# Performance work log

Hardware: AMD Instinct MI355X
Metric: run time of the kernel (lower is better)

The kernel has to match this reference:

```python
import jax, jax.numpy as jnp
import numpy as np

RNN = 400
K_WIN = 10      # num_window_mixtures
N_MIX = 20      # num_mixtures
ALPHA = 80      # alphabet_size
IN2 = RNN + ALPHA + 3  # lstm2/lstm3 input size = 483
MDN_OUT = 1 + 6 * N_MIX  # 121


def setup_inputs() -> dict:
    key = jax.random.key(0)
    ks = jax.random.split(key, 20)
    std = 0.075
    B, T, U = 256, 800, 100
    inp = {
        "trajectory": jax.random.normal(ks[0], (B, T, 3), jnp.float32),
        "char_sequence": jax.random.uniform(ks[1], (B, U, ALPHA), jnp.float32),
        # LSTM1 (input 3)
        "w_ih1": jax.random.normal(ks[2], (4 * RNN, 3), jnp.float32) * std,
        "w_hh1": jax.random.normal(ks[3], (4 * RNN, RNN), jnp.float32) * std,
        "b1": jax.random.normal(ks[4], (4 * RNN,), jnp.float32) * std,
        # LSTM2 (input 483)
        "w_ih2": jax.random.normal(ks[5], (4 * RNN, IN2), jnp.float32) * std,
        "w_hh2": jax.random.normal(ks[6], (4 * RNN, RNN), jnp.float32) * std,
        "b2": jax.random.normal(ks[7], (4 * RNN,), jnp.float32) * std,
        # LSTM3 (input 483)
        "w_ih3": jax.random.normal(ks[8], (4 * RNN, IN2), jnp.float32) * std,
        "w_hh3": jax.random.normal(ks[9], (4 * RNN, RNN), jnp.float32) * std,
        "b3": jax.random.normal(ks[10], (4 * RNN,), jnp.float32) * std,
        # window linear (Graves attention), bias init mean -3.0 std 0.25
        "w_win": jax.random.normal(ks[11], (3 * K_WIN, RNN), jnp.float32) * std,
        "b_win": jax.random.normal(ks[12], (3 * K_WIN,), jnp.float32) * 0.25 - 3.0,
        # MDN head
        "w_mdn": jax.random.normal(ks[13], (MDN_OUT, RNN), jnp.float32) * std,
        "b_mdn": jax.random.normal(ks[14], (MDN_OUT,), jnp.float32) * std,
    }
    return inp


def _lstm_cell(x, h, c, w_ih, w_hh, b):
    # torch.nn.LSTMCell gate order: i, f, g, o
    gates = x @ w_ih.T + h @ w_hh.T + b
    i, f, g, o = jnp.split(gates, 4, axis=-1)
    c_new = jax.nn.sigmoid(f) * c + jax.nn.sigmoid(i) * jnp.tanh(g)
    h_new = jax.nn.sigmoid(o) * jnp.tanh(c_new)
    return h_new, c_new


def reference(trajectory, char_sequence,
              w_ih1, w_hh1, b1, w_ih2, w_hh2, b2, w_ih3, w_hh3, b3,
              w_win, b_win, w_mdn, b_mdn):
    B, T, _ = trajectory.shape
    U = char_sequence.shape[1]
    u = jnp.arange(U, dtype=trajectory.dtype)  # [U]

    def step(carry, x_t):
        h1, c1, h2, c2, h3, c3, kappa = carry
        h1, c1 = _lstm_cell(x_t, h1, c1, w_ih1, w_hh1, b1)
        # Gaussian-window attention
        wp = jnp.exp(h1 @ w_win.T + b_win).reshape(B, 3, K_WIN)
        alpha, beta, dkappa = wp[:, 0], wp[:, 1], wp[:, 2]
        kappa = kappa + dkappa
        # phi: [B, U] = sum_k alpha_k * exp(-beta_k * (kappa_k - u)^2)
        diff = kappa[:, :, None] - u[None, None, :]          # [B, K, U]
        phi = jnp.sum(alpha[:, :, None] * jnp.exp(-beta[:, :, None] * diff * diff), axis=1)
        window = jnp.einsum('bu,bua->ba', phi, char_sequence)  # [B, ALPHA]
        x2 = jnp.concatenate([h1, window, x_t], axis=1)
        h2, c2 = _lstm_cell(x2, h2, c2, w_ih2, w_hh2, b2)
        x3 = jnp.concatenate([h2, window, x_t], axis=1)
        h3, c3 = _lstm_cell(x3, h3, c3, w_ih3, w_hh3, b3)
        out = h3 @ w_mdn.T + b_mdn  # [B, 121]
        return (h1, c1, h2, c2, h3, c3, kappa), out

    z = jnp.zeros((B, RNN), trajectory.dtype)
    kappa0 = jnp.zeros((B, K_WIN), trajectory.dtype)
    carry0 = (z, z, z, z, z, z, kappa0)
    _, outs = jax.lax.scan(step, carry0, jnp.swapaxes(trajectory, 0, 1))  # [T, B, 121]
    return jnp.swapaxes(outs, 0, 1)  # [B, T, 121]
```

## Files before the change

### kernel.cpp

```cpp
#include <hip/hip_runtime.h>
#include <hip/hip_bf16.h>

#define RNNU 400
#define NBATCH 256
#define TT 800
#define UU 100
#define ALW 80
#define KW 10
#define K1 416
#define K2 896
#define NBLK 96
#define NTHR 256

typedef unsigned short u16;
typedef unsigned int u32;
typedef unsigned long long u64;
typedef __attribute__((ext_vector_type(8))) short bfrag;
typedef __attribute__((ext_vector_type(4))) float f4;

constexpr long P1 = (long)NBATCH * K1;
constexpr long P2 = (long)NBATCH * K2;
constexpr long WP1 = 1600L * K1;
constexpr long WP2 = 1600L * K2;
constexpr long WPM = 128L * K1;
constexpr long WPW = 32L * K1;

constexpr size_t OFF_FLAGS = 0;
constexpr size_t OFF_U1 = 16384;
constexpr size_t OFF_U2 = OFF_U1 + (size_t)4 * P1 * 2;
constexpr size_t OFF_U3 = OFF_U2 + (size_t)4 * P2 * 2;
constexpr size_t OFF_W1 = OFF_U3 + (size_t)4 * P2 * 2;
constexpr size_t OFF_W2 = OFF_W1 + (size_t)2 * WP1 * 2;
constexpr size_t OFF_W3 = OFF_W2 + (size_t)2 * WP2 * 2;
constexpr size_t OFF_WM = OFF_W3 + (size_t)2 * WP2 * 2;
constexpr size_t OFF_WW = OFF_WM + (size_t)2 * WPM * 2;
constexpr size_t OFF_PB1 = OFF_WW + (size_t)2 * WPW * 2;
constexpr size_t OFF_PB2 = OFF_PB1 + 6400;
constexpr size_t OFF_PB3 = OFF_PB2 + 6400;
constexpr size_t OFF_C1 = OFF_PB3 + 6400;
constexpr size_t OFF_C2 = OFF_C1 + 409600;
constexpr size_t OFF_C3 = OFF_C2 + 409600;
constexpr size_t OFF_KP = OFF_C3 + 409600;

__device__ __forceinline__ u16 f2b(float x) {
  union { float f; u32 u; } v; v.f = x;
  u32 r = (v.u + 0x7FFFu + ((v.u >> 16) & 1u)) >> 16;
  return (u16)r;
}
__device__ __forceinline__ float b2f(u16 h) {
  union { u32 u; float f; } q; q.u = ((u32)h) << 16; return q.f;
}
__device__ __forceinline__ void wsp2(u16* base, long plane, long idx, float v) {
  u16 hi = f2b(v);
  base[idx] = hi;
  base[plane + idx] = f2b(v - b2f(hi));
}
__device__ __forceinline__ void wsp2c(u16* base, long plane, long idx, float v) {
  u16 hi = f2b(v);
  __hip_atomic_store(base + idx, hi, __ATOMIC_RELAXED, __HIP_MEMORY_SCOPE_AGENT);
  __hip_atomic_store(base + plane + idx, f2b(v - b2f(hi)), __ATOMIC_RELAXED, __HIP_MEMORY_SCOPE_AGENT);
}
__device__ __forceinline__ void st_coh16(u16* p, u16 v) {
  __hip_atomic_store(p, v, __ATOMIC_RELAXED, __HIP_MEMORY_SCOPE_AGENT);
}
__device__ __forceinline__ bfrag ld_frag_coh(const u16* p) {
  u64 lo = __hip_atomic_load((const u64*)p, __ATOMIC_RELAXED, __HIP_MEMORY_SCOPE_AGENT);
  u64 hi = __hip_atomic_load((const u64*)(p + 4), __ATOMIC_RELAXED, __HIP_MEMORY_SCOPE_AGENT);
  union { u64 q[2]; bfrag f; } u; u.q[0] = lo; u.q[1] = hi; return u.f;
}
__device__ __forceinline__ float sigf(float x) { return 1.f / (1.f + __expf(-x)); }
__device__ __forceinline__ float tanhf_(float x) {
  float e = __expf(-2.f * x); return (1.f - e) / (1.f + e);
}

__global__ void prep_kernel(
    const float* __restrict__ w_ih1, const float* __restrict__ w_hh1, const float* __restrict__ b1,
    const float* __restrict__ w_ih2, const float* __restrict__ w_hh2, const float* __restrict__ b2,
    const float* __restrict__ w_ih3, const float* __restrict__ w_hh3, const float* __restrict__ b3,
    const float* __restrict__ w_win, const float* __restrict__ w_mdn,
    const float* __restrict__ traj, char* __restrict__ ws)
{
  u16* W1 = (u16*)(ws + OFF_W1);
  u16* W2 = (u16*)(ws + OFF_W2);
  u16* W3 = (u16*)(ws + OFF_W3);
  u16* WM = (u16*)(ws + OFF_WM);
  u16* WW = (u16*)(ws + OFF_WW);

  const long N1 = WP1, N2 = WP2, N3 = WP2;
  const long N4 = WPM, N5 = WPW, N6 = 4800, N7 = 307200, N8 = 2560, N9 = 4096;
  const long N10 = P1, N11 = (long)NBATCH * RNNU, N12 = (long)NBATCH * RNNU;
  const long total = N1 + N2 + N3 + N4 + N5 + N6 + N7 + N8 + N9 + N10 + N11 + N12;

  for (long i = (long)blockIdx.x * blockDim.x + threadIdx.x; i < total;
       i += (long)gridDim.x * blockDim.x) {
    long j = i;
    if (j < N1) { int n = (int)(j / K1), k = (int)(j % K1);
      int s = (n & 3) * 400 + (n >> 2);
      float v = (k < 3) ? w_ih1[s * 3 + k] : ((k >= 16) ? w_hh1[(long)s * 400 + (k - 16)] : 0.f);
      wsp2(W1, WP1, j, v); continue; } j -= N1;
    if (j < N2) { int n = (int)(j / K2), k = (int)(j % K2);
      int s = (n & 3) * 400 + (n >> 2);
      float v = (k < 483) ? w_ih2[(long)s * 483 + k] : ((k >= 496) ? w_hh2[(long)s * 400 + (k - 496)] : 0.f);
      wsp2(W2, WP2, j, v); continue; } j -= N2;
    if (j < N3) { int n = (int)(j / K2), k = (int)(j % K2);
      int s = (n & 3) * 400 + (n >> 2);
      float v = (k < 483) ? w_ih3[(long)s * 483 + k] : ((k >= 496) ? w_hh3[(long)s * 400 + (k - 496)] : 0.f);
      wsp2(W3, WP2, j, v); continue; } j -= N3;
    if (j < N4) { int n = (int)(j / K1), k = (int)(j % K1);
      float v = (n < 121 && k >= 16) ? w_mdn[(long)n * 400 + (k - 16)] : 0.f;
      wsp2(WM, WPM, j, v); continue; } j -= N4;
    if (j < N5) { int n = (int)(j / K1), k = (int)(j % K1);
      float v = (n < 30 && k < 400) ? w_win[(long)n * 400 + k] : 0.f;
      wsp2(WW, WPW, j, v); continue; } j -= N5;
    if (j < N6) { int w = (int)(j / 1600), n = (int)(j % 1600);
      int s = (n & 3) * 400 + (n >> 2);
      float* pb = (float*)(ws + (w == 0 ? OFF_PB1 : (w == 1 ? OFF_PB2 : OFF_PB3)));
      const float* bb = (w == 0 ? b1 : (w == 1 ? b2 : b3));
      pb[n] = bb[s]; continue; } j -= N6;
    if (j < N7) { ((float*)(ws + OFF_C1))[j] = 0.f; continue; } j -= N7;
    if (j < N8) { ((float*)(ws + OFF_KP))[j] = 0.f; continue; } j -= N8;
    if (j < N9) { ((u32*)(ws + OFF_FLAGS))[j] = 0u; continue; } j -= N9;
    if (j < N10) { int r = (int)(j / K1), k = (int)(j % K1);
      u16* U1 = (u16*)(ws + OFF_U1);
      float v = (k < 3) ? traj[(long)r * 2400 + k] : 0.f;
      wsp2(U1, P1, j, v); continue; } j -= N10;
    if (j < N11) { int r = (int)(j / 400), k = (int)(j % 400);
      u16* U2 = (u16*)(ws + OFF_U2);
      long idx = (long)r * K2 + 496 + k;
      U2[idx] = 0; U2[P2 + idx] = 0; continue; } j -= N11;
    { int r = (int)(j / 400), k = (int)(j % 400);
      u16* U3 = (u16*)(ws + OFF_U3);
      long idx = (long)r * K2 + 496 + k;
      U3[idx] = 0; U3[P2 + idx] = 0; }
  }
}

__device__ __forceinline__ void gridbar(u32* bar, u32 target, int tid) {
  asm volatile("s_waitcnt vmcnt(0)" ::: "memory");
  __syncthreads();
  if (tid == 0) {
    u32 old = __hip_atomic_fetch_add(&bar[0], 1u, __ATOMIC_RELAXED, __HIP_MEMORY_SCOPE_AGENT);
    if (old == target * NBLK - 1u) {
      __hip_atomic_store(&bar[16], target, __ATOMIC_RELAXED, __HIP_MEMORY_SCOPE_AGENT);
    } else {
      while (__hip_atomic_load(&bar[16], __ATOMIC_RELAXED, __HIP_MEMORY_SCOPE_AGENT) < target)
        __builtin_amdgcn_s_sleep(2);
    }
  }
  __syncthreads();
}

template<int NK, int KPAD>
__device__ __forceinline__ void gemm_gate_tile(
    int rt, int ct, const u16* __restrict__ Abase, long APS,
    const u16* __restrict__ Wbase, long WPS,
    const float* __restrict__ pbias, float* __restrict__ cst,
    u16* __restrict__ hd0, int st0, long ps0,
    u16* __restrict__ hd1, int st1, long ps1,
    float* __restrict__ ldsb, int lane)
{
  const int r0 = rt * 32, c0 = ct * 80;
  f4 acc[2][5];
#pragma unroll
  for (int a = 0; a < 2; a++)
#pragma unroll
    for (int b = 0; b < 5; b++) acc[a][b] = (f4)(0.f);

  const long aoff = (long)(r0 + (lane & 15)) * KPAD + ((lane >> 4) * 8);
  const long woff = (long)(c0 + (lane & 15)) * KPAD + ((lane >> 4) * 8);
  const u16* Ah0 = Abase + aoff;
  const u16* Ah1 = Ah0 + 16 * KPAD;
  const u16* Al0 = Abase + APS + aoff;
  const u16* Al1 = Al0 + 16 * KPAD;
  const u16* Wh = Wbase + woff;
  const u16* Wl = Wbase + WPS + woff;

#pragma unroll
  for (int kb = 0; kb < NK; ++kb) {
    bfrag a0 = ld_frag_coh(Ah0 + kb * 32);
    bfrag a1 = ld_frag_coh(Ah1 + kb * 32);
#pragma unroll
    for (int cf = 0; cf < 5; ++cf) {
      bfrag wh = *(const bfrag*)(Wh + (long)cf * 16 * KPAD + kb * 32);
      bfrag wl = *(const bfrag*)(Wl + (long)cf * 16 * KPAD + kb * 32);
      acc[0][cf] = __builtin_amdgcn_mfma_f32_16x16x32_bf16(a0, wh, acc[0][cf], 0, 0, 0);
      acc[1][cf] = __builtin_amdgcn_mfma_f32_16x16x32_bf16(a1, wh, acc[1][cf], 0, 0, 0);
      acc[0][cf] = __builtin_amdgcn_mfma_f32_16x16x32_bf16(a0, wl, acc[0][cf], 0, 0, 0);
      acc[1][cf] = __builtin_amdgcn_mfma_f32_16x16x32_bf16(a1, wl, acc[1][cf], 0, 0, 0);
    }
  }
#pragma unroll
  for (int kb = 0; kb < NK; ++kb) {
    bfrag a0 = ld_frag_coh(Al0 + kb * 32);
    bfrag a1 = ld_frag_coh(Al1 + kb * 32);
#pragma unroll
    for (int cf = 0; cf < 5; ++cf) {
      bfrag wh = *(const bfrag*)(Wh + (long)cf * 16 * KPAD + kb * 32);
      acc[0][cf] = __builtin_amdgcn_mfma_f32_16x16x32_bf16(a0, wh, acc[0][cf], 0, 0, 0);
      acc[1][cf] = __builtin_amdgcn_mfma_f32_16x16x32_bf16(a1, wh, acc[1][cf], 0, 0, 0);
    }
  }
  const int cl = lane & 15, rq = lane >> 4;
#pragma unroll
  for (int rf = 0; rf < 2; ++rf)
#pragma unroll
    for (int cf = 0; cf < 5; ++cf) {
      float bias = pbias[c0 + cf * 16 + cl];
#pragma unroll
      for (int r = 0; r < 4; ++r)
        ldsb[(rf * 16 + rq * 4 + r) * 80 + cf * 16 + cl] = acc[rf][cf][r] + bias;
    }
  asm volatile("s_waitcnt lgkmcnt(0)" ::: "memory");
#pragma unroll
  for (int q = 0; q < 10; ++q) {
    int idx = q * 64 + lane;
    int rl = idx / 20, ul = idx % 20;
    float gi = ldsb[rl * 80 + 4 * ul + 0];
    float gf = ldsb[rl * 80 + 4 * ul + 1];
    float gg = ldsb[rl * 80 + 4 * ul + 2];
    float go = ldsb[rl * 80 + 4 * ul + 3];
    long row = r0 + rl; int unit = ct * 20 + ul;
    long ci = row * 400 + unit;
    float cn = sigf(gf) * cst[ci] + sigf(gi) * tanhf_(gg);
    cst[ci] = cn;
    float hv = sigf(go) * tanhf_(cn);
    u16 hh = f2b(hv);
    u16 hl = f2b(hv - b2f(hh));
    long i0 = row * st0 + unit;
    st_coh16(hd0 + i0, hh); st_coh16(hd0 + ps0 + i0, hl);
    if (hd1) { long i1 = row * st1 + unit; st_coh16(hd1 + i1, hh); st_coh16(hd1 + ps1 + i1, hl); }
  }
}

__device__ __forceinline__ void mdn_tile(
    int mt, const u16* __restrict__ Abase, long APS,
    const u16* __restrict__ Wm, long WPS,
    const float* __restrict__ b_mdn, float* __restrict__ out, int tcol, int lane)
{
  const int r0 = mt * 16;
  f4 acc[8];
#pragma unroll
  for (int c = 0; c < 8; c++) acc[c] = (f4)(0.f);
  const long aoff = (long)(r0 + (lane & 15)) * K2 + ((lane >> 4) * 8);
  const long woff = (long)(lane & 15) * K1 + ((lane >> 4) * 8);
  const u16* Ah = Abase + aoff;
  const u16* Al = Abase + APS + aoff;
  const u16* Wh = Wm + woff;
  const u16* Wl = Wm + WPS + woff;
#pragma unroll
  for (int kb = 0; kb < 13; ++kb) {
    bfrag a = ld_frag_coh(Ah + kb * 32);
#pragma unroll
    for (int cf = 0; cf < 8; ++cf) {
      bfrag wh = *(const bfrag*)(Wh + (long)cf * 16 * K1 + kb * 32);
      bfrag wl = *(const bfrag*)(Wl + (long)cf * 16 * K1 + kb * 32);
      acc[cf] = __builtin_amdgcn_mfma_f32_16x16x32_bf16(a, wh, acc[cf], 0, 0, 0);
      acc[cf] = __builtin_amdgcn_mfma_f32_16x16x32_bf16(a, wl, acc[cf], 0, 0, 0);
    }
  }
#pragma unroll
  for (int kb = 0; kb < 13; ++kb) {
    bfrag a = ld_frag_coh(Al + kb * 32);
#pragma unroll
    for (int cf = 0; cf < 8; ++cf) {
      bfrag wh = *(const bfrag*)(Wh + (long)cf * 16 * K1 + kb * 32);
      acc[cf] = __builtin_amdgcn_mfma_f32_16x16x32_bf16(a, wh, acc[cf], 0, 0, 0);
    }
  }
  const int cl = lane & 15, rq = lane >> 4;
#pragma unroll
  for (int cf = 0; cf < 8; ++cf) {
    int col = cf * 16 + cl;
    if (col < 121) {
      float bias = b_mdn[col];
#pragma unroll
      for (int r = 0; r < 4; ++r) {
        long row = r0 + rq * 4 + r;
        out[(row * TT + tcol) * 121 + col] = acc[cf][r] + bias;
      }
    }
  }
}

__global__ void __launch_bounds__(NTHR) handw_kernel(
    const float* __restrict__ traj, const float* __restrict__ chars,
    const float* __restrict__ b_win, const float* __restrict__ b_mdn,
    float* __restrict__ out, char* __restrict__ ws)
{
  u32* bar = (u32*)(ws + OFF_FLAGS);
  u16* U1b = (u16*)(ws + OFF_U1);
  u16* U2b = (u16*)(ws + OFF_U2);
  u16* U3b = (u16*)(ws + OFF_U3);
  const u16* W1 = (const u16*)(ws + OFF_W1);
  const u16* W2 = (const u16*)(ws + OFF_W2);
  const u16* W3 = (const u16*)(ws + OFF_W3);
  const u16* WM = (const u16*)(ws + OFF_WM);
  const u16* WW = (const u16*)(ws + OFF_WW);
  const float* PB1 = (const float*)(ws + OFF_PB1);
  const float* PB2 = (const float*)(ws + OFF_PB2);
  const float* PB3 = (const float*)(ws + OFF_PB3);
  float* C1 = (float*)(ws + OFF_C1);
  float* C2 = (float*)(ws + OFF_C2);
  float* C3 = (float*)(ws + OFF_C3);
  float* KP = (float*)(ws + OFF_KP);

  __shared__ float ldseb[2][32 * 80];
  __shared__ float ldswp[16 * 32];
  __shared__ float ldsal[16 * KW];
  __shared__ float ldsbe[16 * KW];
  __shared__ float ldskp[16 * KW];
  __shared__ float ldsphi[16 * UU];

  const int bid = blockIdx.x, tid = threadIdx.x;
  const int wid = tid >> 6, lane = tid & 63;
  u32 epoch = 0;
  const int gtile = (wid < 2 && bid < 80) ? (wid * 80 + bid) : -1;
  const int rt = (gtile >= 0) ? gtile / 20 : 0;
  const int ct = (gtile >= 0) ? gtile % 20 : 0;

  for (int t = 0; t < TT; ++t) {
    const int p = t & 1;
    u16* U1p = U1b + (size_t)p * 2 * P1;
    u16* U1n = U1b + (size_t)(p ^ 1) * 2 * P1;
    u16* U2p = U2b + (size_t)p * 2 * P2;
    u16* U2n = U2b + (size_t)(p ^ 1) * 2 * P2;
    u16* U3p = U3b + (size_t)p * 2 * P2;
    u16* U3n = U3b + (size_t)(p ^ 1) * 2 * P2;

    if (gtile >= 0)
      gemm_gate_tile<13, K1>(rt, ct, U1p, P1, W1, WP1, PB1, C1,
                             U1n + 16, K1, P1, U2p, K2, P2, ldseb[wid], lane);
    if (t > 0 && wid == 0 && bid >= 80 && bid < 96)
      mdn_tile(bid - 80, U3p + 480, P2, WM, WPM, b_mdn, out, t - 1, lane);
    gridbar(bar, ++epoch, tid);

    if (bid < 16) {
      const int r0 = bid * 16;
      if (wid == 0) {
        f4 wacc[2]; wacc[0] = (f4)(0.f); wacc[1] = (f4)(0.f);
        const long aoff = (long)(r0 + (lane & 15)) * K2 + ((lane >> 4) * 8);
        const long woff = (long)(lane & 15) * K1 + ((lane >> 4) * 8);
        const u16* Ah = U2p + aoff;
        const u16* Al = U2p + P2 + aoff;
        const u16* Wh = WW + woff;
        const u16* Wl = WW + WPW + woff;
#pragma unroll
        for (int kb = 0; kb < 13; ++kb) {
          bfrag a = ld_frag_coh(Ah + kb * 32);
          bfrag b0h = *(const bfrag*)(Wh + kb * 32);
          bfrag b0l = *(const bfrag*)(Wl + kb * 32);
          bfrag b1h = *(const bfrag*)(Wh + 16 * K1 + kb * 32);
          bfrag b1l = *(const bfrag*)(Wl + 16 * K1 + kb * 32);
          wacc[0] = __builtin_amdgcn_mfma_f32_16x16x32_bf16(a, b0h, wacc[0], 0, 0, 0);
          wacc[0] = __builtin_amdgcn_mfma_f32_16x16x32_bf16(a, b0l, wacc[0], 0, 0, 0);
          wacc[1] = __builtin_amdgcn_mfma_f32_16x16x32_bf16(a, b1h, wacc[1], 0, 0, 0);
          wacc[1] = __builtin_amdgcn_mfma_f32_16x16x32_bf16(a, b1l, wacc[1], 0, 0, 0);
        }
#pragma unroll
        for (int kb = 0; kb < 13; ++kb) {
          bfrag a = ld_frag_coh(Al + kb * 32);
          bfrag b0h = *(const bfrag*)(Wh + kb * 32);
          bfrag b1h = *(const bfrag*)(Wh + 16 * K1 + kb * 32);
          wacc[0] = __builtin_amdgcn_mfma_f32_16x16x32_bf16(a, b0h, wacc[0], 0, 0, 0);
          wacc[1] = __builtin_amdgcn_mfma_f32_16x16x32_bf16(a, b1h, wacc[1], 0, 0, 0);
        }
        const int cl = lane & 15, rq = lane >> 4;
#pragma unroll
        for (int cf = 0; cf < 2; ++cf) {
          int col = cf * 16 + cl;
          float bias = (col < 30) ? b_win[col] : 0.f;
#pragma unroll
          for (int r = 0; r < 4; ++r)
            ldswp[(rq * 4 + r) * 32 + col] = wacc[cf][r] + bias;
        }
      }
      __syncthreads();
      if (tid < 160) {
        int r = tid / 10, k = tid % 10; int row = r0 + r;
        float kap = KP[row * 10 + k] + __expf(ldswp[r * 32 + 20 + k]);
        KP[row * 10 + k] = kap;
        ldskp[r * 10 + k] = kap;
        ldsal[r * 10 + k] = __expf(ldswp[r * 32 + k]);
        ldsbe[r * 10 + k] = __expf(ldswp[r * 32 + 10 + k]);
      } else if (tid < 208) {
        int q = tid - 160; int r = q / 3, c = q % 3; int row = r0 + r;
        float xv = traj[((long)row * TT + t) * 3 + c];
        wsp2c(U2p, P2, (long)row * K2 + 480 + c, xv);
        wsp2c(U3p, P2, (long)row * K2 + 480 + c, xv);
        if (t + 1 < TT)
          wsp2c(U1n, P1, (long)row * K1 + c, traj[((long)row * TT + t + 1) * 3 + c]);
      }
      __syncthreads();
      {
        int r = tid & 15, uq = tid >> 4;
        for (int u = uq; u < UU; u += 16) {
          float s = 0.f;
#pragma unroll
          for (int k = 0; k < KW; ++k) {
            float d = ldskp[r * 10 + k] - (float)u;
            s += ldsal[r * 10 + k] * __expf(-ldsbe[r * 10 + k] * d * d);
          }
          ldsphi[r * UU + u] = s;
        }
      }
      __syncthreads();
      {
        int r = tid >> 4, d0 = tid & 15; int row = r0 + r;
        float w[5] = {0.f, 0.f, 0.f, 0.f, 0.f};
        const float* cb = chars + (long)row * UU * ALW;
#pragma unroll 4
        for (int u = 0; u < UU; ++u) {
          float ph = ldsphi[r * UU + u];
#pragma unroll
          for (int jj = 0; jj < 5; ++jj) w[jj] += ph * cb[u * ALW + d0 + 16 * jj];
        }
#pragma unroll
        for (int jj = 0; jj < 5; ++jj) {
          int d = d0 + 16 * jj;
          wsp2c(U2p, P2, (long)row * K2 + 400 + d, w[jj]);
          wsp2c(U3p, P2, (long)row * K2 + 400 + d, w[jj]);
        }
      }
    }
    gridbar(bar, ++epoch, tid);

    if (gtile >= 0)
      gemm_gate_tile<28, K2>(rt, ct, U2p, P2, W2, WP2, PB2, C2,
                             U3p, K2, P2, U2n + 496, K2, P2, ldseb[wid], lane);
    gridbar(bar, ++epoch, tid);

    if (gtile >= 0)
      gemm_gate_tile<28, K2>(rt, ct, U3p, P2, W3, WP2, PB3, C3,
                             U3n + 496, K2, P2, (u16*)nullptr, 0, 0, ldseb[wid], lane);
    gridbar(bar, ++epoch, tid);
  }
  if (wid == 0 && bid >= 80 && bid < 96)
    mdn_tile(bid - 80, U3b + 480, P2, WM, WPM, b_mdn, out, TT - 1, lane);
}

extern "C" void kernel_launch(void* const* d_in, const int* in_sizes, int n_in,
                              void* d_out, int out_size, void* d_ws, size_t ws_size,
                              hipStream_t stream) {
  const float* traj   = (const float*)d_in[0];
  const float* chars  = (const float*)d_in[1];
  const float* w_ih1  = (const float*)d_in[2];
  const float* w_hh1  = (const float*)d_in[3];
  const float* b1     = (const float*)d_in[4];
  const float* w_ih2  = (const float*)d_in[5];
  const float* w_hh2  = (const float*)d_in[6];
  const float* b2     = (const float*)d_in[7];
  const float* w_ih3  = (const float*)d_in[8];
  const float* w_hh3  = (const float*)d_in[9];
  const float* b3     = (const float*)d_in[10];
  const float* w_win  = (const float*)d_in[11];
  const float* b_win  = (const float*)d_in[12];
  const float* w_mdn  = (const float*)d_in[13];
  const float* b_mdn  = (const float*)d_in[14];
  float* outp = (float*)d_out;
  char* wsp = (char*)d_ws;

  prep_kernel<<<dim3(8192), dim3(256), 0, stream>>>(
      w_ih1, w_hh1, b1, w_ih2, w_hh2, b2, w_ih3, w_hh3, b3, w_win, w_mdn, traj, wsp);

  void* kargs[] = { (void*)&traj, (void*)&chars, (void*)&b_win, (void*)&b_mdn,
                    (void*)&outp, (void*)&wsp };
  hipError_t err = hipLaunchCooperativeKernel((void*)handw_kernel, dim3(NBLK), dim3(NTHR),
                                              kargs, 0, stream);
  if (err != hipSuccess) {
    handw_kernel<<<dim3(NBLK), dim3(NTHR), 0, stream>>>(traj, chars, b_win, b_mdn, outp, wsp);
  }
}
```

Measured before the change: 340.4 ms.

## Stage activation panels into LDS per block and reshape grid to 80 blocks

Each block now cooperatively loads its 32-row activation panel (hi and lo planes) from global memory into a 112KB LDS buffer with coherent loads, and the two gate waves then read A fragments from LDS. Before, each wave fetched A straight from global. The grid shrinks from 96 to 80 blocks, with each block covering one row tile and two column tiles across its two waves. The MDN head moves onto blocks 16-31, running alongside the window stage with its own LDS staging. Staging adds a __syncthreads and a serial global-to-LDS copy on every phase, the large LDS allocation limits occupancy, and tanh gets an input clamp.

```diff
diff --git a/kernel.cpp b/kernel.cpp
--- a/kernel.cpp
+++ b/kernel.cpp
@@ -9,7 +9,7 @@
 #define KW 10
 #define K1 416
 #define K2 896
-#define NBLK 96
+#define NBLK 80
 #define NTHR 256
 
 typedef unsigned short u16;
@@ -63,13 +63,13 @@
 __device__ __forceinline__ void st_coh16(u16* p, u16 v) {
   __hip_atomic_store(p, v, __ATOMIC_RELAXED, __HIP_MEMORY_SCOPE_AGENT);
 }
-__device__ __forceinline__ bfrag ld_frag_coh(const u16* p) {
-  u64 lo = __hip_atomic_load((const u64*)p, __ATOMIC_RELAXED, __HIP_MEMORY_SCOPE_AGENT);
-  u64 hi = __hip_atomic_load((const u64*)(p + 4), __ATOMIC_RELAXED, __HIP_MEMORY_SCOPE_AGENT);
-  union { u64 q[2]; bfrag f; } u; u.q[0] = lo; u.q[1] = hi; return u.f;
+__device__ __forceinline__ void coh16(u64* a, u64* b, const u16* p) {
+  *a = __hip_atomic_load((const u64*)p, __ATOMIC_RELAXED, __HIP_MEMORY_SCOPE_AGENT);
+  *b = __hip_atomic_load((const u64*)(p + 4), __ATOMIC_RELAXED, __HIP_MEMORY_SCOPE_AGENT);
 }
 __device__ __forceinline__ float sigf(float x) { return 1.f / (1.f + __expf(-x)); }
 __device__ __forceinline__ float tanhf_(float x) {
+  x = fminf(fmaxf(x, -30.f), 30.f);
   float e = __expf(-2.f * x); return (1.f - e) / (1.f + e);
 }
 
@@ -150,35 +150,103 @@
   __syncthreads();
 }
 
+template<int KPAD>
+__device__ __forceinline__ void stage_gates(const u16* U, long PS, int r0, char* lds, int tid) {
+  constexpr int CPR = KPAD / 8;
+  constexpr int CPP = 32 * CPR;
+  constexpr int PLB = 32 * KPAD * 2;
+  constexpr int TOT = 2 * CPP;
+  const u16* s0 = U + (long)r0 * KPAD;
+  int c = tid;
+  while (c < TOT) {
+    u64 va[8], vb[8];
+#pragma unroll
+    for (int j = 0; j < 8; ++j) {
+      int cc = c + j * NTHR;
+      if (cc < TOT) {
+        int P = cc >= CPP; int r = cc - (P ? CPP : 0);
+        coh16(&va[j], &vb[j], s0 + (P ? PS : 0) + (long)r * 8);
+      }
+    }
+#pragma unroll
+    for (int j = 0; j < 8; ++j) {
+      int cc = c + j * NTHR;
+      if (cc < TOT) {
+        int P = cc >= CPP; int r = cc - (P ? CPP : 0);
+        int db = (P ? PLB : 0) + r * 16;
+        *(u64*)(lds + db) = va[j];
+        *(u64*)(lds + db + 8) = vb[j];
+      }
+    }
+    c += 8 * NTHR;
+  }
+}
+
+__device__ __forceinline__ void stage_slice(const u16* U, long PS, int r0, int coloff,
+                                            char* lds, int tid) {
+  constexpr int CPR = 52;
+  constexpr int CPP = 16 * CPR;
+  constexpr int PLB = 16 * 416 * 2;
+  constexpr int TOT = 2 * CPP;
+  int c = tid;
+  while (c < TOT) {
+    u64 va[8], vb[8];
+#pragma unroll
+    for (int j = 0; j < 8; ++j) {
+      int cc = c + j * NTHR;
+      if (cc < TOT) {
+        int P = cc >= CPP; int r = cc - (P ? CPP : 0);
+        int row = r / CPR, col = r % CPR;
+        coh16(&va[j], &vb[j], U + (P ? PS : 0) + (long)(r0 + row) * K2 + coloff + col * 8);
+      }
+    }
+#pragma unroll
+    for (int j = 0; j < 8; ++j) {
+      int cc = c + j * NTHR;
+      if (cc < TOT) {
+        int P = cc >= CPP; int r = cc - (P ? CPP : 0);
+        int db = (P ? PLB : 0) + r * 16;
+        *(u64*)(lds + db) = va[j];
+        *(u64*)(lds + db + 8) = vb[j];
+      }
+    }
+    c += 8 * NTHR;
+  }
+}
+
+template<int ROWB>
+__device__ __forceinline__ bfrag ldsfrag(const char* pl, int row, int cb) {
+  return *(const bfrag*)(pl + row * ROWB + cb);
+}
+
 template<int NK, int KPAD>
-__device__ __forceinline__ void gemm_gate_tile(
-    int rt, int ct, const u16* __restrict__ Abase, long APS,
+__device__ __forceinline__ void gemm_gate_lds(
+    int r0, int ct, const char* panel,
     const u16* __restrict__ Wbase, long WPS,
     const float* __restrict__ pbias, float* __restrict__ cst,
     u16* __restrict__ hd0, int st0, long ps0,
     u16* __restrict__ hd1, int st1, long ps1,
     float* __restrict__ ldsb, int lane)
 {
-  const int r0 = rt * 32, c0 = ct * 80;
+  const int c0 = ct * 80;
   f4 acc[2][5];
 #pragma unroll
   for (int a = 0; a < 2; a++)
 #pragma unroll
     for (int b = 0; b < 5; b++) acc[a][b] = (f4)(0.f);
 
-  const long aoff = (long)(r0 + (lane & 15)) * KPAD + ((lane >> 4) * 8);
   const long woff = (long)(c0 + (lane & 15)) * KPAD + ((lane >> 4) * 8);
-  const u16* Ah0 = Abase + aoff;
-  const u16* Ah1 = Ah0 + 16 * KPAD;
-  const u16* Al0 = Abase + APS + aoff;
-  const u16* Al1 = Al0 + 16 * KPAD;
   const u16* Wh = Wbase + woff;
   const u16* Wl = Wbase + WPS + woff;
+  const int rA = lane & 15;
+  const int cb0 = ((lane >> 4) * 8) * 2;
+  const char* p0 = panel;
+  const char* p1 = panel + 32 * KPAD * 2;
 
 #pragma unroll
   for (int kb = 0; kb < NK; ++kb) {
-    bfrag a0 = ld_frag_coh(Ah0 + kb * 32);
-    bfrag a1 = ld_frag_coh(Ah1 + kb * 32);
+    bfrag a0 = ldsfrag<KPAD * 2>(p0, rA, cb0 + kb * 64);
+    bfrag a1 = ldsfrag<KPAD * 2>(p0, rA + 16, cb0 + kb * 64);
 #pragma unroll
     for (int cf = 0; cf < 5; ++cf) {
       bfrag wh = *(const bfrag*)(Wh + (long)cf * 16 * KPAD + kb * 32);
@@ -191,8 +259,8 @@
   }
 #pragma unroll
   for (int kb = 0; kb < NK; ++kb) {
-    bfrag a0 = ld_frag_coh(Al0 + kb * 32);
-    bfrag a1 = ld_frag_coh(Al1 + kb * 32);
+    bfrag a0 = ldsfrag<KPAD * 2>(p1, rA, cb0 + kb * 64);
+    bfrag a1 = ldsfrag<KPAD * 2>(p1, rA + 16, cb0 + kb * 64);
 #pragma unroll
     for (int cf = 0; cf < 5; ++cf) {
       bfrag wh = *(const bfrag*)(Wh + (long)cf * 16 * KPAD + kb * 32);
@@ -232,24 +300,24 @@
   }
 }
 
-__device__ __forceinline__ void mdn_tile(
-    int mt, const u16* __restrict__ Abase, long APS,
-    const u16* __restrict__ Wm, long WPS,
+__device__ __forceinline__ void mdn_lds(
+    int mt, const char* panel, const u16* __restrict__ Wm, long WPS,
     const float* __restrict__ b_mdn, float* __restrict__ out, int tcol, int lane)
 {
   const int r0 = mt * 16;
   f4 acc[8];
 #pragma unroll
   for (int c = 0; c < 8; c++) acc[c] = (f4)(0.f);
-  const long aoff = (long)(r0 + (lane & 15)) * K2 + ((lane >> 4) * 8);
   const long woff = (long)(lane & 15) * K1 + ((lane >> 4) * 8);
-  const u16* Ah = Abase + aoff;
-  const u16* Al = Abase + APS + aoff;
   const u16* Wh = Wm + woff;
   const u16* Wl = Wm + WPS + woff;
+  const int rA = lane & 15;
+  const int cb0 = ((lane >> 4) * 8) * 2;
+  const char* p0 = panel;
+  const char* p1 = panel + 13312;
 #pragma unroll
   for (int kb = 0; kb < 13; ++kb) {
-    bfrag a = ld_frag_coh(Ah + kb * 32);
+    bfrag a = ldsfrag<832>(p0, rA, cb0 + kb * 64);
 #pragma unroll
     for (int cf = 0; cf < 8; ++cf) {
       bfrag wh = *(const bfrag*)(Wh + (long)cf * 16 * K1 + kb * 32);
@@ -260,7 +328,7 @@
   }
 #pragma unroll
   for (int kb = 0; kb < 13; ++kb) {
-    bfrag a = ld_frag_coh(Al + kb * 32);
+    bfrag a = ldsfrag<832>(p1, rA, cb0 + kb * 64);
 #pragma unroll
     for (int cf = 0; cf < 8; ++cf) {
       bfrag wh = *(const bfrag*)(Wh + (long)cf * 16 * K1 + kb * 32);
@@ -304,6 +372,7 @@
   float* C3 = (float*)(ws + OFF_C3);
   float* KP = (float*)(ws + OFF_KP);
 
+  __shared__ __align__(16) char panel[114688];
   __shared__ float ldseb[2][32 * 80];
   __shared__ float ldswp[16 * 32];
   __shared__ float ldsal[16 * KW];
@@ -314,9 +383,10 @@
   const int bid = blockIdx.x, tid = threadIdx.x;
   const int wid = tid >> 6, lane = tid & 63;
   u32 epoch = 0;
-  const int gtile = (wid < 2 && bid < 80) ? (wid * 80 + bid) : -1;
-  const int rt = (gtile >= 0) ? gtile / 20 : 0;
-  const int ct = (gtile >= 0) ? gtile % 20 : 0;
+  const int rt = bid / 10, cp = bid % 10;
+  const int r0 = rt * 32;
+  const int ct = cp * 2 + (wid & 1);
+  const bool gw = (wid < 2);
 
   for (int t = 0; t < TT; ++t) {
     const int p = t & 1;
@@ -327,26 +397,29 @@
     u16* U3p = U3b + (size_t)p * 2 * P2;
     u16* U3n = U3b + (size_t)(p ^ 1) * 2 * P2;
 
-    if (gtile >= 0)
-      gemm_gate_tile<13, K1>(rt, ct, U1p, P1, W1, WP1, PB1, C1,
-                             U1n + 16, K1, P1, U2p, K2, P2, ldseb[wid], lane);
-    if (t > 0 && wid == 0 && bid >= 80 && bid < 96)
-      mdn_tile(bid - 80, U3p + 480, P2, WM, WPM, b_mdn, out, t - 1, lane);
+    stage_gates<K1>(U1p, P1, r0, panel, tid);
+    __syncthreads();
+    if (gw)
+      gemm_gate_lds<13, K1>(r0, ct, panel, W1, WP1, PB1, C1,
+                            U1n + 16, K1, P1, U2p, K2, P2, ldseb[wid], lane);
     gridbar(bar, ++epoch, tid);
 
     if (bid < 16) {
-      const int r0 = bid * 16;
+      const int rb0 = bid * 16;
+      stage_slice(U2p, P2, rb0, 0, panel, tid);
+      __syncthreads();
       if (wid == 0) {
         f4 wacc[2]; wacc[0] = (f4)(0.f); wacc[1] = (f4)(0.f);
-        const long aoff = (long)(r0 + (lane & 15)) * K2 + ((lane >> 4) * 8);
         const long woff = (long)(lane & 15) * K1 + ((lane >> 4) * 8);
-        const u16* Ah = U2p + aoff;
-        const u16* Al = U2p + P2 + aoff;
         const u16* Wh = WW + woff;
         const u16* Wl = WW + WPW + woff;
+        const int rA = lane & 15;
+        const int cb0 = ((lane >> 4) * 8) * 2;
+        const char* p0 = panel;
+        const char* p1 = panel + 13312;
 #pragma unroll
         for (int kb = 0; kb < 13; ++kb) {
-          bfrag a = ld_frag_coh(Ah + kb * 32);
+          bfrag a = ldsfrag<832>(p0, rA, cb0 + kb * 64);
           bfrag b0h = *(const bfrag*)(Wh + kb * 32);
           bfrag b0l = *(const bfrag*)(Wl + kb * 32);
           bfrag b1h = *(const bfrag*)(Wh + 16 * K1 + kb * 32);
@@ -358,7 +431,7 @@
         }
 #pragma unroll
         for (int kb = 0; kb < 13; ++kb) {
-          bfrag a = ld_frag_coh(Al + kb * 32);
+          bfrag a = ldsfrag<832>(p1, rA, cb0 + kb * 64);
           bfrag b0h = *(const bfrag*)(Wh + kb * 32);
           bfrag b1h = *(const bfrag*)(Wh + 16 * K1 + kb * 32);
           wacc[0] = __builtin_amdgcn_mfma_f32_16x16x32_bf16(a, b0h, wacc[0], 0, 0, 0);
@@ -376,14 +449,14 @@
       }
       __syncthreads();
       if (tid < 160) {
-        int r = tid / 10, k = tid % 10; int row = r0 + r;
+        int r = tid / 10, k = tid % 10; int row = rb0 + r;
         float kap = KP[row * 10 + k] + __expf(ldswp[r * 32 + 20 + k]);
         KP[row * 10 + k] = kap;
         ldskp[r * 10 + k] = kap;
         ldsal[r * 10 + k] = __expf(ldswp[r * 32 + k]);
         ldsbe[r * 10 + k] = __expf(ldswp[r * 32 + 10 + k]);
       } else if (tid < 208) {
-        int q = tid - 160; int r = q / 3, c = q % 3; int row = r0 + r;
+        int q = tid - 160; int r = q / 3, c = q % 3; int row = rb0 + r;
         float xv = traj[((long)row * TT + t) * 3 + c];
         wsp2c(U2p, P2, (long)row * K2 + 480 + c, xv);
         wsp2c(U3p, P2, (long)row * K2 + 480 + c, xv);
@@ -405,7 +478,7 @@
       }
       __syncthreads();
       {
-        int r = tid >> 4, d0 = tid & 15; int row = r0 + r;
+        int r = tid >> 4, d0 = tid & 15; int row = rb0 + r;
         float w[5] = {0.f, 0.f, 0.f, 0.f, 0.f};
         const float* cb = chars + (long)row * UU * ALW;
 #pragma unroll 4
@@ -421,21 +494,36 @@
           wsp2c(U3p, P2, (long)row * K2 + 400 + d, w[jj]);
         }
       }
+    } else if (bid < 32 && t > 0) {
+      const int mt = bid - 16;
+      stage_slice(U3p, P2, mt * 16, 480, panel, tid);
+      __syncthreads();
+      if (wid == 0)
+        mdn_lds(mt, panel, WM, WPM, b_mdn, out, t - 1, lane);
     }
     gridbar(bar, ++epoch, tid);
 
-    if (gtile >= 0)
-      gemm_gate_tile<28, K2>(rt, ct, U2p, P2, W2, WP2, PB2, C2,
-                             U3p, K2, P2, U2n + 496, K2, P2, ldseb[wid], lane);
+    stage_gates<K2>(U2p, P2, r0, panel, tid);
+    __syncthreads();
+    if (gw)
+      gemm_gate_lds<28, K2>(r0, ct, panel, W2, WP2, PB2, C2,
+                            U3p, K2, P2, U2n + 496, K2, P2, ldseb[wid], lane);
     gridbar(bar, ++epoch, tid);
 
-    if (gtile >= 0)
-      gemm_gate_tile<28, K2>(rt, ct, U3p, P2, W3, WP2, PB3, C3,
-                             U3n + 496, K2, P2, (u16*)nullptr, 0, 0, ldseb[wid], lane);
+    stage_gates<K2>(U3p, P2, r0, panel, tid);
+    __syncthreads();
+    if (gw)
+      gemm_gate_lds<28, K2>(r0, ct, panel, W3, WP2, PB3, C3,
+                            U3n + 496, K2, P2, (u16*)nullptr, 0, 0, ldseb[wid], lane);
     gridbar(bar, ++epoch, tid);
   }
-  if (wid == 0 && bid >= 80 && bid < 96)
-    mdn_tile(bid - 80, U3b + 480, P2, WM, WPM, b_mdn, out, TT - 1, lane);
+  if (bid >= 16 && bid < 32) {
+    const int mt = bid - 16;
+    stage_slice(U3b, P2, mt * 16, 480, panel, tid);
+    __syncthreads();
+    if (wid == 0)
+      mdn_lds(mt, panel, WM, WPM, b_mdn, out, TT - 1, lane);
+  }
 }
 
 extern "C" void kernel_launch(void* const* d_in, const int* in_sizes, int n_in,
```

New measurement: 319.4 ms. -6.2%, faster.
